# Kernel tuning notes

Hardware: AMD Instinct MI355X
Metric: run time of the kernel (lower is better)

Reference implementation:

```python
import jax, jax.numpy as jnp
import numpy as np

B, T, H = 2, 512, 256


def setup_inputs() -> dict:
    key = jax.random.key(0)
    k1, k2, k3, k4, k5 = jax.random.split(key, 5)
    scale = 1.0 / np.sqrt(H)
    Q = jax.random.normal(k1, (B, T, H), dtype=jnp.float32)
    K = jax.random.normal(k2, (B, T, H), dtype=jnp.float32)
    # torch nn.Linear weights: y = x @ W.T, W shape [out, in]
    Wq = jax.random.normal(k3, (H, H), dtype=jnp.float32) * scale
    Wk = jax.random.normal(k4, (H, H), dtype=jnp.float32) * scale
    v = jax.random.normal(k5, (H,), dtype=jnp.float32) * scale  # Linear(H,1) weight
    return {"Q": Q, "K": K, "Wq": Wq, "Wk": Wk, "v": v}


def reference(Q, K, Wq, Wk, v):
    # Project queries and keys: [B,T,H]
    Qp = jnp.einsum("bth,oh->bto", Q, Wq)
    Kp = jnp.einsum("bsh,oh->bso", K, Wk)
    # Additive (Bahdanau) scores: tanh over broadcast sum -> [B,T,T,H], then v-proj -> [B,T,T]
    e = jnp.tanh(Qp[:, :, None, :] + Kp[:, None, :, :])
    scores = jnp.einsum("btsh,h->bts", e, v)
    # Causal mask: query t may only attend to keys s <= t
    mask = jnp.tril(jnp.ones((T, T), dtype=bool))
    scores = jnp.where(mask[None, :, :], scores, jnp.float32(-1e9))
    alpha = jax.nn.softmax(scores, axis=-1)
    # Weighted sum of (raw) K values: [B,T,H]
    ctx = jnp.einsum("bts,bsh->bth", alpha, K)
    return ctx, alpha
```

## Files before the change

kernel.cpp:

```cpp
#include <hip/hip_runtime.h>

#define BB 2
#define TT 512
#define HH 256
#define NBT (BB * TT)

#define C2LOG2E 2.8853900817779268f
#define LOG2E   1.4426950408889634f

typedef __attribute__((ext_vector_type(8))) short short8;
typedef __attribute__((ext_vector_type(4))) float f32x4;

__device__ __forceinline__ unsigned short f2bf(float f) {
    unsigned u = __float_as_uint(f);
    unsigned r = u + 0x7fffu + ((u >> 16) & 1u);
    return (unsigned short)(r >> 16);
}

__global__ __launch_bounds__(256) void prep_kernel(
    const float* __restrict__ Q, const float* __restrict__ K,
    const float* __restrict__ Wq, const float* __restrict__ Wk,
    unsigned short* __restrict__ Qb, unsigned short* __restrict__ Kb,
    unsigned short* __restrict__ Wqb, unsigned short* __restrict__ Wkb)
{
    int bid = blockIdx.x, tid = threadIdx.x;
    const float* src;
    unsigned short* dst;
    int base;
    if (bid < 256)      { src = Q;  dst = Qb;  base = bid * 1024; }
    else if (bid < 512) { src = K;  dst = Kb;  base = (bid - 256) * 1024; }
    else if (bid < 576) { src = Wq; dst = Wqb; base = (bid - 512) * 1024; }
    else                { src = Wk; dst = Wkb; base = (bid - 576) * 1024; }
    int i = base + tid * 4;
    float4 x4 = *reinterpret_cast<const float4*>(src + i);
    ushort4 o4;
    o4.x = f2bf(x4.x); o4.y = f2bf(x4.y); o4.z = f2bf(x4.z); o4.w = f2bf(x4.w);
    *reinterpret_cast<ushort4*>(dst + i) = o4;
}

__global__ __launch_bounds__(256) void proj_mfma_kernel(
    const unsigned short* __restrict__ Qb, const unsigned short* __restrict__ Kb,
    const unsigned short* __restrict__ Wqb, const unsigned short* __restrict__ Wkb,
    float* __restrict__ Eq, float* __restrict__ EkT)
{
    int wid_g = blockIdx.x * 4 + (threadIdx.x >> 6);
    int lane = threadIdx.x & 63;
    int btile = wid_g >> 3;
    int otile = wid_g & 7;
    bool isK = (btile >= 32);
    int bt0 = (btile & 31) * 32;
    int o0 = otile * 32;
    const unsigned short* X = isK ? Kb : Qb;
    const unsigned short* W = isK ? Wkb : Wqb;

    int rsel = lane & 15;
    int ksel = (lane >> 4) * 8;

    f32x4 c00 = {0.f,0.f,0.f,0.f}, c01 = {0.f,0.f,0.f,0.f};
    f32x4 c10 = {0.f,0.f,0.f,0.f}, c11 = {0.f,0.f,0.f,0.f};

#pragma unroll
    for (int kb = 0; kb < 8; ++kb) {
        int ko = kb * 32 + ksel;
        short8 a0 = *reinterpret_cast<const short8*>(X + (bt0 + rsel) * HH + ko);
        short8 a1 = *reinterpret_cast<const short8*>(X + (bt0 + 16 + rsel) * HH + ko);
        short8 b0 = *reinterpret_cast<const short8*>(W + (o0 + rsel) * HH + ko);
        short8 b1 = *reinterpret_cast<const short8*>(W + (o0 + 16 + rsel) * HH + ko);
        c00 = __builtin_amdgcn_mfma_f32_16x16x32_bf16(a0, b0, c00, 0, 0, 0);
        c01 = __builtin_amdgcn_mfma_f32_16x16x32_bf16(a0, b1, c01, 0, 0, 0);
        c10 = __builtin_amdgcn_mfma_f32_16x16x32_bf16(a1, b0, c10, 0, 0, 0);
        c11 = __builtin_amdgcn_mfma_f32_16x16x32_bf16(a1, b1, c11, 0, 0, 0);
    }

    int rbase = (lane >> 4) * 4;
    int cbase = lane & 15;
#pragma unroll
    for (int mi = 0; mi < 2; ++mi) {
#pragma unroll
        for (int ni = 0; ni < 2; ++ni) {
            f32x4 cc = (mi == 0) ? (ni == 0 ? c00 : c01)
                                 : (ni == 0 ? c10 : c11);
#pragma unroll
            for (int j = 0; j < 4; ++j) {
                float e = __builtin_amdgcn_exp2f(cc[j] * C2LOG2E);
                int r = bt0 + mi * 16 + rbase + j;
                int o = o0 + ni * 16 + cbase;
                if (!isK)
                    Eq[r * HH + o] = e;
                else
                    EkT[((o >> 2) * NBT + r) * 4 + (o & 3)] = e;
            }
        }
    }
}

__global__ __launch_bounds__(512, 8) void attn_kernel(
    const float* __restrict__ Eq, const float* __restrict__ EkT,
    const float* __restrict__ Kraw, const float* __restrict__ v,
    float* __restrict__ ctx, float* __restrict__ alpha)
{
    __shared__ float eq_sh[HH];
    __shared__ float v2_sh[HH];
    __shared__ float al_sh[TT];
    __shared__ float red[8];
    __shared__ float4 cred[8][64];

    int bt = blockIdx.x;
    int b = bt / TT;
    int idx = bt % TT;
    int t = (idx < 256) ? idx : 767 - idx;
    int btr = b * TT + t;
    int tid = threadIdx.x;

    if (tid < HH) {
        eq_sh[tid] = Eq[btr * HH + tid];
        v2_sh[tid] = -2.0f * v[tid];
    }
    __syncthreads();

    float sc = 0.f;
    if (tid <= t) {
        const float4* ek = reinterpret_cast<const float4*>(EkT) + (b * TT + tid);
        const float4* q4p = reinterpret_cast<const float4*>(eq_sh);
        const float4* v4p = reinterpret_cast<const float4*>(v2_sh);
#pragma unroll 4
        for (int h4 = 0; h4 < HH / 4; ++h4) {
            float4 e4 = ek[h4 * NBT];
            float4 q4 = q4p[h4];
            float4 vv = v4p[h4];
            float r0 = __builtin_amdgcn_rcpf(__builtin_fmaf(q4.x, e4.x, 1.f));
            float r1 = __builtin_amdgcn_rcpf(__builtin_fmaf(q4.y, e4.y, 1.f));
            float r2 = __builtin_amdgcn_rcpf(__builtin_fmaf(q4.z, e4.z, 1.f));
            float r3 = __builtin_amdgcn_rcpf(__builtin_fmaf(q4.w, e4.w, 1.f));
            sc = __builtin_fmaf(vv.x, r0, sc);
            sc = __builtin_fmaf(vv.y, r1, sc);
            sc = __builtin_fmaf(vv.z, r2, sc);
            sc = __builtin_fmaf(vv.w, r3, sc);
        }
    }

    float e = (tid <= t) ? __builtin_amdgcn_exp2f(sc * LOG2E) : 0.f;
    float ssum = e;
#pragma unroll
    for (int off = 32; off > 0; off >>= 1)
        ssum += __shfl_xor(ssum, off);
    if ((tid & 63) == 0) red[tid >> 6] = ssum;
    __syncthreads();
    float denom = (red[0] + red[1]) + (red[2] + red[3])
                + (red[4] + red[5]) + (red[6] + red[7]);
    float a0 = e * __builtin_amdgcn_rcpf(denom);

    al_sh[tid] = a0;
    alpha[btr * TT + tid] = a0;
    __syncthreads();

    int hc = tid & 63, sg = tid >> 6;
    const float4* kb4 = reinterpret_cast<const float4*>(Kraw + b * TT * HH) + hc;
    float4 acc4 = {0.f, 0.f, 0.f, 0.f};
    for (int s = sg; s <= t; s += 8) {
        float4 k4 = kb4[s * 64];
        float  al = al_sh[s];
        acc4.x = __builtin_fmaf(al, k4.x, acc4.x);
        acc4.y = __builtin_fmaf(al, k4.y, acc4.y);
        acc4.z = __builtin_fmaf(al, k4.z, acc4.z);
        acc4.w = __builtin_fmaf(al, k4.w, acc4.w);
    }
    cred[sg][hc] = acc4;
    __syncthreads();
    if (sg == 0) {
        float4 out = {0.f, 0.f, 0.f, 0.f};
#pragma unroll
        for (int g = 0; g < 8; ++g) {
            float4 cc = cred[g][hc];
            out.x += cc.x; out.y += cc.y; out.z += cc.z; out.w += cc.w;
        }
        reinterpret_cast<float4*>(ctx + btr * HH)[hc] = out;
    }
}

extern "C" void kernel_launch(void* const* d_in, const int* in_sizes, int n_in,
                              void* d_out, int out_size, void* d_ws, size_t ws_size,
                              hipStream_t stream) {
    const float* Q  = (const float*)d_in[0];
    const float* K  = (const float*)d_in[1];
    const float* Wq = (const float*)d_in[2];
    const float* Wk = (const float*)d_in[3];
    const float* v  = (const float*)d_in[4];

    float* ctx   = (float*)d_out;
    float* alpha = (float*)d_out + NBT * HH;

    float* Eq  = (float*)d_ws;
    float* EkT = Eq + NBT * HH;
    unsigned short* Qb  = (unsigned short*)(EkT + NBT * HH);
    unsigned short* Kb  = Qb + NBT * HH;
    unsigned short* Wqb = Kb + NBT * HH;
    unsigned short* Wkb = Wqb + HH * HH;

    prep_kernel<<<640, 256, 0, stream>>>(Q, K, Wq, Wk, Qb, Kb, Wqb, Wkb);
    proj_mfma_kernel<<<128, 256, 0, stream>>>(Qb, Kb, Wqb, Wkb, Eq, EkT);
    attn_kernel<<<NBT, 512, 0, stream>>>(Eq, EkT, K, v, ctx, alpha);
}
```

Before: 39.66 us.

## Fuse bf16 conversion into projection MFMA kernel and shrink per-wave tiles

Removes the separate prep kernel that converted Q, K, Wq, Wk to bf16 and instead loads fp32 directly in the projection kernel, converting to bf16 in registers before each MFMA. Each wave now computes a single 16x16 output tile instead of 32x32, and the grid grows from 128 to 512 blocks to spread the work across more CUs. This saves one kernel launch and a round-trip of the bf16 copies through memory, but each wave loads twice as many bytes (fp32), and with smaller tiles inputs are re-read more often across waves.

```diff
diff --git a/kernel.cpp b/kernel.cpp
--- a/kernel.cpp
+++ b/kernel.cpp
@@ -17,80 +17,56 @@
     return (unsigned short)(r >> 16);
 }
 
-__global__ __launch_bounds__(256) void prep_kernel(
-    const float* __restrict__ Q, const float* __restrict__ K,
-    const float* __restrict__ Wq, const float* __restrict__ Wk,
-    unsigned short* __restrict__ Qb, unsigned short* __restrict__ Kb,
-    unsigned short* __restrict__ Wqb, unsigned short* __restrict__ Wkb)
-{
-    int bid = blockIdx.x, tid = threadIdx.x;
-    const float* src;
-    unsigned short* dst;
-    int base;
-    if (bid < 256)      { src = Q;  dst = Qb;  base = bid * 1024; }
-    else if (bid < 512) { src = K;  dst = Kb;  base = (bid - 256) * 1024; }
-    else if (bid < 576) { src = Wq; dst = Wqb; base = (bid - 512) * 1024; }
-    else                { src = Wk; dst = Wkb; base = (bid - 576) * 1024; }
-    int i = base + tid * 4;
-    float4 x4 = *reinterpret_cast<const float4*>(src + i);
-    ushort4 o4;
-    o4.x = f2bf(x4.x); o4.y = f2bf(x4.y); o4.z = f2bf(x4.z); o4.w = f2bf(x4.w);
-    *reinterpret_cast<ushort4*>(dst + i) = o4;
+__device__ __forceinline__ short8 load_cvt8(const float* __restrict__ p) {
+    float4 x0 = *reinterpret_cast<const float4*>(p);
+    float4 x1 = *reinterpret_cast<const float4*>(p + 4);
+    short8 r;
+    r[0] = (short)f2bf(x0.x); r[1] = (short)f2bf(x0.y);
+    r[2] = (short)f2bf(x0.z); r[3] = (short)f2bf(x0.w);
+    r[4] = (short)f2bf(x1.x); r[5] = (short)f2bf(x1.y);
+    r[6] = (short)f2bf(x1.z); r[7] = (short)f2bf(x1.w);
+    return r;
 }
 
 __global__ __launch_bounds__(256) void proj_mfma_kernel(
-    const unsigned short* __restrict__ Qb, const unsigned short* __restrict__ Kb,
-    const unsigned short* __restrict__ Wqb, const unsigned short* __restrict__ Wkb,
+    const float* __restrict__ Q, const float* __restrict__ K,
+    const float* __restrict__ Wq, const float* __restrict__ Wk,
     float* __restrict__ Eq, float* __restrict__ EkT)
 {
     int wid_g = blockIdx.x * 4 + (threadIdx.x >> 6);
     int lane = threadIdx.x & 63;
-    int btile = wid_g >> 3;
-    int otile = wid_g & 7;
-    bool isK = (btile >= 32);
-    int bt0 = (btile & 31) * 32;
-    int o0 = otile * 32;
-    const unsigned short* X = isK ? Kb : Qb;
-    const unsigned short* W = isK ? Wkb : Wqb;
+    int btile = wid_g >> 4;
+    int otile = wid_g & 15;
+    bool isK = (btile >= 64);
+    int bt0 = (btile & 63) * 16;
+    int o0 = otile * 16;
+    const float* X = isK ? K : Q;
+    const float* W = isK ? Wk : Wq;
 
     int rsel = lane & 15;
     int ksel = (lane >> 4) * 8;
 
-    f32x4 c00 = {0.f,0.f,0.f,0.f}, c01 = {0.f,0.f,0.f,0.f};
-    f32x4 c10 = {0.f,0.f,0.f,0.f}, c11 = {0.f,0.f,0.f,0.f};
+    const float* xp = X + (bt0 + rsel) * HH + ksel;
+    const float* wp = W + (o0 + rsel) * HH + ksel;
 
-#pragma unroll
+    f32x4 acc = {0.f, 0.f, 0.f, 0.f};
+#pragma unroll 2
     for (int kb = 0; kb < 8; ++kb) {
-        int ko = kb * 32 + ksel;
-        short8 a0 = *reinterpret_cast<const short8*>(X + (bt0 + rsel) * HH + ko);
-        short8 a1 = *reinterpret_cast<const short8*>(X + (bt0 + 16 + rsel) * HH + ko);
-        short8 b0 = *reinterpret_cast<const short8*>(W + (o0 + rsel) * HH + ko);
-        short8 b1 = *reinterpret_cast<const short8*>(W + (o0 + 16 + rsel) * HH + ko);
-        c00 = __builtin_amdgcn_mfma_f32_16x16x32_bf16(a0, b0, c00, 0, 0, 0);
-        c01 = __builtin_amdgcn_mfma_f32_16x16x32_bf16(a0, b1, c01, 0, 0, 0);
-        c10 = __builtin_amdgcn_mfma_f32_16x16x32_bf16(a1, b0, c10, 0, 0, 0);
-        c11 = __builtin_amdgcn_mfma_f32_16x16x32_bf16(a1, b1, c11, 0, 0, 0);
+        short8 a = load_cvt8(xp + kb * 32);
+        short8 b = load_cvt8(wp + kb * 32);
+        acc = __builtin_amdgcn_mfma_f32_16x16x32_bf16(a, b, acc, 0, 0, 0);
     }
 
-    int rbase = (lane >> 4) * 4;
-    int cbase = lane & 15;
+    int rbase = bt0 + (lane >> 4) * 4;
+    int o = o0 + (lane & 15);
 #pragma unroll
-    for (int mi = 0; mi < 2; ++mi) {
-#pragma unroll
-        for (int ni = 0; ni < 2; ++ni) {
-            f32x4 cc = (mi == 0) ? (ni == 0 ? c00 : c01)
-                                 : (ni == 0 ? c10 : c11);
-#pragma unroll
-            for (int j = 0; j < 4; ++j) {
-                float e = __builtin_amdgcn_exp2f(cc[j] * C2LOG2E);
-                int r = bt0 + mi * 16 + rbase + j;
-                int o = o0 + ni * 16 + cbase;
-                if (!isK)
-                    Eq[r * HH + o] = e;
-                else
-                    EkT[((o >> 2) * NBT + r) * 4 + (o & 3)] = e;
-            }
-        }
+    for (int j = 0; j < 4; ++j) {
+        float e = __builtin_amdgcn_exp2f(acc[j] * C2LOG2E);
+        int r = rbase + j;
+        if (!isK)
+            Eq[r * HH + o] = e;
+        else
+            EkT[((o >> 2) * NBT + r) * 4 + (o & 3)] = e;
     }
 }
 
@@ -192,12 +168,7 @@
 
     float* Eq  = (float*)d_ws;
     float* EkT = Eq + NBT * HH;
-    unsigned short* Qb  = (unsigned short*)(EkT + NBT * HH);
-    unsigned short* Kb  = Qb + NBT * HH;
-    unsigned short* Wqb = Kb + NBT * HH;
-    unsigned short* Wkb = Wqb + HH * HH;
 
-    prep_kernel<<<640, 256, 0, stream>>>(Q, K, Wq, Wk, Qb, Kb, Wqb, Wkb);
-    proj_mfma_kernel<<<128, 256, 0, stream>>>(Qb, Kb, Wqb, Wkb, Eq, EkT);
+    proj_mfma_kernel<<<512, 256, 0, stream>>>(Q, K, Wq, Wk, Eq, EkT);
     attn_kernel<<<NBT, 512, 0, stream>>>(Eq, EkT, K, v, ctx, alpha);
 }
```

Result: faster. 37.51 us (-5.4%).
